# Kernel tuning notes

Hardware: AMD Instinct MI355X
Metric: run time of the kernel (lower is better)

Reference implementation:

```python
import jax, jax.numpy as jnp
import numpy as np

NL, NS, NE = 16, 256, 100   # nlatent, nspatial, n_embd
B, P, T = 2, 2, 12


def _xavier(key, shape):
    # torch xavier_uniform: fan_in = shape[1]*prod(rest), fan_out = shape[0]*prod(rest)
    rf = int(np.prod(shape[2:])) if len(shape) > 2 else 1
    fan_in, fan_out = shape[1] * rf, shape[0] * rf
    b = float(np.sqrt(6.0 / (fan_in + fan_out)))
    return jax.random.uniform(key, shape, jnp.float32, -b, b)


def setup_inputs() -> dict:
    key = jax.random.key(0)
    ks = jax.random.split(key, 8)
    x = jax.random.normal(ks[0], (B, P, T, NL, NS), jnp.float32)
    K = _xavier(ks[1], (NS, NS, NL))
    Q = _xavier(ks[2], (NS, NS, NL))
    V = _xavier(ks[3], (NS, NS, NL))
    Aoo = jnp.ones((NS, NS), jnp.float32)
    # Ann is initialized to zeros in the module; use nonzero values so the
    # clamped geometric recurrence over time is actually exercised.
    Ann = jax.random.uniform(ks[4], (NE,), jnp.float32, -0.9, 0.9)
    Aon = _xavier(ks[5], (NS, NS, NE))
    Ano = _xavier(ks[6], (NS, NS, NE))
    w = jnp.ones((NS,), jnp.float32) / NS
    return {"x": x, "K": K, "Q": Q, "V": V, "Aoo": Aoo,
            "Ann": Ann, "Aon": Aon, "Ano": Ano, "w": w}


def reference(x, K, Q, V, Aoo, Ann, Aon, Ano, w):
    # kvt[B,p,T,X,Y] = sum_{x,c} Q[Y,x,c] K[X,x,c] x[B,p,T,c,x]
    kvt = jnp.einsum('Yxc,Xxc,BpTcx->BpTXY', Q, K, x)
    Aon_c = jnp.clip(Aon, -1.0, 1.0)
    Ano_c = jnp.clip(Ano, -1.0, 1.0)

    # t = T-1 term (elementwise Aoo) and t = T-2 term
    h = Aoo[None, None, None] * kvt[:, :, -1:]
    h = h + jnp.einsum('xyn,XYn,BpTXY->BpTxy', Aon_c, Ano_c, kvt[:, :, -2:-1])

    nT = x.shape[2]
    # Ann sequence used in the loop: A_2 = Ann (raw), A_{j+1} = clip(A_j * Ann)
    def step(a, _):
        return jnp.clip(a * Ann, -1.0, 1.0), a
    _, A_seq = jax.lax.scan(step, Ann, None, length=nT - 2)  # [T-2, n], A_seq[j-2]=A_j

    # loop index j=2..T-1 touches time slice t = T-1-j, i.e. t = T-3 .. 0
    s = jnp.einsum('XYn,BpJXY->BpJn', Ano_c, kvt[:, :, :nT - 2])  # J = t in 0..T-3
    A_t = A_seq[::-1]                       # align A_j with time index t = T-1-j
    s2 = jnp.einsum('Jn,BpJn->Bpn', A_t, s)
    h = h + jnp.einsum('xyn,Bpn->Bpxy', Aon_c, s2)[:, :, None]  # [B,p,1,x,y]

    q = jnp.einsum('Xxc,Bpcx->BpcX', V, x[:, :, -1])
    y = jnp.einsum('x,BpcX,BpTXx->BpTc', w, q, h)  # [B,p,1,c]
    return y
```

## Files before the change

### kernel.cpp

```cpp
#include <hip/hip_runtime.h>
#include <hip/hip_fp16.h>


using f32x4 = __attribute__((ext_vector_type(4))) float;
using half8 = __attribute__((ext_vector_type(8))) _Float16;
using half4 = __attribute__((ext_vector_type(4))) _Float16;

#define KVT_STRIDE 3145728ull
#define KS 4

__device__ inline float clip1(float v) { return fminf(fmaxf(v, -1.f), 1.f); }

__device__ inline half8 mul8(uint4 a, uint4 b) {
    half8 x = __builtin_bit_cast(half8, a);
    half8 y = __builtin_bit_cast(half8, b);
    return x * y;
}

__device__ __forceinline__ void gl_lds16(const void* g, void* l) {
    __builtin_amdgcn_global_load_lds(
        (const __attribute__((address_space(1))) void*)g,
        (__attribute__((address_space(3))) void*)l, 16, 0, 0);
}

__global__ void prep_kernel(const float* __restrict__ K, const float* __restrict__ Q,
                            const float* __restrict__ xin,
                            __half* __restrict__ Kh, __half* __restrict__ Qh,
                            __half* __restrict__ u_t)
{
    int b = blockIdx.x, t = threadIdx.x;
    if (b < 512) {
        bool isK = (b < 256);
        int bb = isK ? b : b - 256;
        size_t base = (size_t)bb * 4096 + t * 16;
        const f32x4* src = (const f32x4*)((isK ? K : Q) + base);
        __half* dst = (isK ? Kh : Qh) + base;
        #pragma unroll
        for (int j = 0; j < 2; ++j) {
            f32x4 v0 = src[j * 2], v1 = src[j * 2 + 1];
            half8 h;
            h[0] = (_Float16)v0.x; h[1] = (_Float16)v0.y;
            h[2] = (_Float16)v0.z; h[3] = (_Float16)v0.w;
            h[4] = (_Float16)v1.x; h[5] = (_Float16)v1.y;
            h[6] = (_Float16)v1.z; h[7] = (_Float16)v1.w;
            *(half8*)(dst + j * 8) = h;
        }
    } else {
        int bt = b - 512;
        const float* src = xin + (size_t)bt * 4096;
        int xx = t;
        half8 lo, hi;
        #pragma unroll
        for (int c = 0; c < 8; ++c)  lo[c] = (_Float16)src[c * 256 + xx];
        #pragma unroll
        for (int c = 0; c < 8; ++c)  hi[c] = (_Float16)src[(c + 8) * 256 + xx];
        half8* dst = (half8*)(u_t + (size_t)bt * 4096 + xx * 16);
        dst[0] = lo; dst[1] = hi;
    }
}

__global__ __launch_bounds__(256, 4) void gemm_kvt(
    const __half* __restrict__ Kh, const __half* __restrict__ Qh,
    const __half* __restrict__ u_t, __half* __restrict__ kvtp)
{
    __shared__ __half As[2][128][32];
    __shared__ __half Bs[2][128][32];
    __shared__ __half u_s[1024];

    int bid = blockIdx.x;
    int work = (bid & 7) * 96 + (bid >> 3);
    int kc = work / 192;
    int rem = work - kc * 192;
    int tile = rem / 48;
    int bt = rem - tile * 48;
    int Xb = (tile >> 1) * 128, Yb = (tile & 1) * 128;
    int kbase = kc * 1024;

    int tid = threadIdx.x;
    if (tid < 128)
        *(uint4*)&u_s[tid * 8] = *(const uint4*)(u_t + (size_t)bt * 4096 + kbase + tid * 8);
    __syncthreads();

    int wave = tid >> 6, lane = tid & 63;

    int arow = tid >> 1;
    int apair = (tid & 1) * 2;
    const __half* gA = Kh + (size_t)(Xb + arow) * 4096 + kbase + apair * 8;
    int aswz = (arow >> 1) & 3;
    int asb0 = ((apair + 0) ^ aswz) << 4;
    int asb1 = ((apair + 1) ^ aswz) << 4;

    int srow = lane >> 2;
    int sk = ((lane & 3) ^ ((srow >> 1) & 3)) << 3;
    const __half* gB = Qh + (size_t)(Yb + wave * 16 + srow) * 4096 + kbase + sk;

    int wr = (wave >> 1) * 64, wc = (wave & 1) * 64;
    int lrow = lane & 15, kg = lane >> 4;
    int fb = (kg * 16) ^ (((lrow >> 1) & 3) << 4);

    f32x4 acc[4][4];
    f32x4 zero = {0.f, 0.f, 0.f, 0.f};
    #pragma unroll
    for (int m = 0; m < 4; ++m)
        #pragma unroll
        for (int n = 0; n < 4; ++n) acc[m][n] = zero;

    #define ISSUE_B(s, buf)                                                    \
        do {                                                                   \
            _Pragma("unroll")                                                  \
            for (int i_ = 0; i_ < 2; ++i_)                                     \
                gl_lds16(gB + (size_t)(i_ * 64) * 4096 + (s) * 32,             \
                         &Bs[buf][i_ * 64 + wave * 16][0]);                    \
        } while (0)

    #define WRITE_A(s, r0, r1, buf)                                            \
        do {                                                                   \
            uint4 uv0 = *(const uint4*)&u_s[(s) * 32 + apair * 8];             \
            uint4 uv1 = *(const uint4*)&u_s[(s) * 32 + apair * 8 + 8];         \
            *(half8*)((char*)&As[buf][arow][0] + asb0) = mul8(r0, uv0);        \
            *(half8*)((char*)&As[buf][arow][0] + asb1) = mul8(r1, uv1);        \
        } while (0)

    #define COMPUTE(cur)                                                       \
        do {                                                                   \
            half8 af[4], bf[4];                                                \
            _Pragma("unroll")                                                  \
            for (int m = 0; m < 4; ++m)                                        \
                af[m] = *(const half8*)((const char*)&As[cur][wr + m * 16 + lrow][0] + fb); \
            _Pragma("unroll")                                                  \
            for (int n = 0; n < 4; ++n)                                        \
                bf[n] = *(const half8*)((const char*)&Bs[cur][wc + n * 16 + lrow][0] + fb); \
            _Pragma("unroll")                                                  \
            for (int m = 0; m < 4; ++m)                                        \
                _Pragma("unroll")                                              \
                for (int n = 0; n < 4; ++n)                                    \
                    acc[m][n] = __builtin_amdgcn_mfma_f32_16x16x32_f16(af[m], bf[n], acc[m][n], 0, 0, 0); \
        } while (0)

    #define STEP(s, c0, c1, i0, i1, cur)                                       \
        do {                                                                   \
            if ((s) < 31) asm volatile("s_waitcnt vmcnt(4) lgkmcnt(0)" ::: "memory"); \
            else          asm volatile("s_waitcnt vmcnt(0) lgkmcnt(0)" ::: "memory"); \
            __builtin_amdgcn_s_barrier();                                      \
            __builtin_amdgcn_sched_barrier(0);                                 \
            COMPUTE(cur);                                                      \
            asm volatile("s_waitcnt lgkmcnt(0)" ::: "memory");                 \
            __builtin_amdgcn_s_barrier();                                      \
            __builtin_amdgcn_sched_barrier(0);                                 \
            if ((s) + 2 < 32) {                                                \
                const __half* a_ = gA + ((s) + 2) * 32;                        \
                i0 = *(const uint4*)a_;                                        \
                i1 = *(const uint4*)(a_ + 8);                                  \
                ISSUE_B((s) + 2, cur);                                         \
            }                                                                  \
            if ((s) + 1 < 32) WRITE_A((s) + 1, c0, c1, (cur) ^ 1);             \
        } while (0)

    uint4 aP0, aP1, aC0, aC1;
    aP0 = *(const uint4*)gA;
    aP1 = *(const uint4*)(gA + 8);
    ISSUE_B(0, 0);
    aC0 = *(const uint4*)(gA + 32);
    aC1 = *(const uint4*)(gA + 40);
    ISSUE_B(1, 1);
    WRITE_A(0, aP0, aP1, 0);

    #pragma unroll
    for (int s = 0; s < 32; s += 2) {
        STEP(s,     aC0, aC1, aP0, aP1, 0);
        STEP(s + 1, aP0, aP1, aC0, aC1, 1);
    }
    #undef STEP
    #undef COMPUTE
    #undef WRITE_A
    #undef ISSUE_B

    __half* outp = kvtp + (size_t)kc * KVT_STRIDE + (size_t)bt * 65536;
    int row0 = Xb + wr + kg * 4;
    int col0 = Yb + wc + lrow;
    #pragma unroll
    for (int m = 0; m < 4; ++m)
        #pragma unroll
        for (int n = 0; n < 4; ++n)
            #pragma unroll
            for (int rr = 0; rr < 4; ++rr)
                outp[(size_t)(row0 + m * 16 + rr) * 256 + col0 + n * 16] =
                    __float2half(acc[m][n][rr]);
}

__global__ __launch_bounds__(256) void mid_kernel(
    const float* __restrict__ Ano, const __half* __restrict__ kvtp,
    const float* __restrict__ V, const float* __restrict__ xin,
    const float* __restrict__ Aon, const float* __restrict__ wv,
    float* __restrict__ Sp, float* __restrict__ R, float* __restrict__ W2p)
{
    __shared__ __align__(16) char smem[75328];
    int b = blockIdx.x, tid = threadIdx.x;

    if (b < 512) {
        float* anoT = (float*)smem;
        float (*kvt_s)[128] = (float(*)[128])(smem + 52800);
        int cb = b;
        int k0 = cb * 128;

        {
            const f32x4* src = (const f32x4*)(Ano + (size_t)k0 * 100);
            for (int i = tid; i < 3200; i += 256) {
                f32x4 f = __builtin_nontemporal_load(src + i);
                int e = i * 4;
                int k = e / 100;
                int n = e - k * 100;
                #pragma unroll
                for (int j = 0; j < 4; ++j) {
                    int nn = n + j, kk2 = k;
                    if (nn >= 100) { nn -= 100; ++kk2; }
                    anoT[nn * 132 + kk2] = clip1(f[j]);
                }
            }
        }
        {
            for (int idx = tid; idx < 5632; idx += 256) {
                int rI = idx >> 7, k = idx & 127;
                int bpr = rI / 11, Jr = rI - bpr * 11;
                size_t off = (size_t)(bpr * 12 + Jr) * 65536 + k0 + k;
                float v = 0.f;
                #pragma unroll
                for (int c = 0; c < KS; ++c)
                    v += __half2float(kvtp[(size_t)c * KVT_STRIDE + off]);
                kvt_s[rI][k] = v;
            }
        }
        __syncthreads();

        int lane = tid & 63;
        int bp = tid >> 6;
        bool has2 = lane < 36;
        float acc0[11], acc1[11];
        #pragma unroll
        for (int J = 0; J < 11; ++J) { acc0[J] = 0.f; acc1[J] = 0.f; }

        const float* a0p = anoT + lane * 132;
        const float* a1p = anoT + (64 + lane) * 132;
        for (int k = 0; k < 128; k += 4) {
            f32x4 kv[11];
            #pragma unroll
            for (int J = 0; J < 11; ++J)
                kv[J] = *(const f32x4*)&kvt_s[bp * 11 + J][k];
            f32x4 a0v = *(const f32x4*)(a0p + k);
            f32x4 a1v = {0.f, 0.f, 0.f, 0.f};
            if (has2) a1v = *(const f32x4*)(a1p + k);
            #pragma unroll
            for (int kk = 0; kk < 4; ++kk) {
                #pragma unroll
                for (int J = 0; J < 11; ++J) {
                    acc0[J] += kv[J][kk] * a0v[kk];
                    acc1[J] += kv[J][kk] * a1v[kk];
                }
            }
        }
        float* outb = Sp + ((size_t)cb * 4 + bp) * 1100;
        #pragma unroll
        for (int J = 0; J < 11; ++J) {
            outb[J * 100 + lane] = acc0[J];
            if (has2) outb[J * 100 + 64 + lane] = acc1[J];
        }
    } else if (b < 768) {
        float* vrow = (float*)smem;
        int X = b - 512;
        {
            const float4* src = (const float4*)(V + (size_t)X * 4096);
            float4* dst = (float4*)vrow;
            for (int i = tid; i < 1024; i += 256) dst[i] = src[i];
        }
        __syncthreads();
        int bp = tid >> 6, c = (tid >> 2) & 15, g = tid & 3;
        const float* xl = xin + ((size_t)(bp * 12) + 11) * 4096 + c * 256;
        float p = 0.f;
        #pragma unroll 4
        for (int x = g * 64; x < g * 64 + 64; ++x)
            p += xl[x] * vrow[x * 16 + c];
        p += __shfl_xor(p, 1);
        p += __shfl_xor(p, 2);
        if (g == 0) R[((size_t)bp * 256 + X) * 16 + c] = p;
    } else {
        int idx = b - 768;
        int X = idx >> 1, h = idx & 1;
        int g = h * 2 + (tid >> 7), n = tid & 127;
        if (n < 100) {
            const float* base = Aon + (size_t)X * 25600 + (size_t)g * 6400 + n;
            float acc = 0.f;
            for (int bb = 0; bb < 64; ++bb)
                acc += wv[g * 64 + bb] * clip1(__builtin_nontemporal_load(base + (size_t)bb * 100));
            W2p[((size_t)g * 256 + X) * 100 + n] = acc;
        }
    }
}

__global__ void reduce_s(const float* __restrict__ Sp, float* __restrict__ Sq,
                         float* __restrict__ out)
{
    int bid = blockIdx.x;
    int t = threadIdx.x;
    if (bid == 0 && t < 64) out[t] = 0.f;
    int qq = bid & 3, idx = bid >> 2;
    int bp = idx / 11, J = idx - bp * 11;
    if (t >= 100) return;
    float acc = 0.f;
    for (int c = qq * 128; c < qq * 128 + 128; ++c)
        acc += Sp[((size_t)c * 4 + bp) * 1100 + J * 100 + t];
    Sq[(size_t)(qq * 44 + idx) * 100 + t] = acc;
}

__global__ __launch_bounds__(256) void hw_kernel(const float* __restrict__ Aoo,
                                                 const float* __restrict__ wv,
                                                 const __half* __restrict__ kvtp,
                                                 const float* __restrict__ W2p,
                                                 const float* __restrict__ Sq,
                                                 const float* __restrict__ Ann,
                                                 const float* __restrict__ R,
                                                 float* __restrict__ out)
{
    __shared__ float yp[4][16];
    __shared__ float c2s[128];
    int bp = blockIdx.x >> 6, Xg = blockIdx.x & 63;
    int tid = threadIdx.x;

    if (tid < 128) {
        int n = tid;
        float r = 0.f;
        if (n < 100) {
            float S[11];
            #pragma unroll
            for (int J = 0; J < 11; ++J) {
                float s = 0.f;
                #pragma unroll
                for (int qq = 0; qq < 4; ++qq)
                    s += Sq[(size_t)(qq * 44 + bp * 11 + J) * 100 + n];
                S[J] = s;
            }
            float a = Ann[n];
            float seq[10];
            float v = a;
            seq[0] = v;
            #pragma unroll
            for (int s2 = 1; s2 < 10; ++s2) { v = clip1(v * a); seq[s2] = v; }
            r = S[10];
            #pragma unroll
            for (int J = 0; J < 10; ++J)
                r += seq[9 - J] * S[J];
        }
        c2s[n] = r;
    }
    __syncthreads();

    int wave = tid >> 6, lane = tid & 63;
    int X = Xg * 4 + wave;
    size_t base = (size_t)(bp * 12 + 11) * 65536 + (size_t)X * 256;
    const float* ao = Aoo + (size_t)X * 256;
    float red = 0.f;
    #pragma unroll
    for (int qq = 0; qq < 4; ++qq) {
        int xx = qq * 64 + lane;
        float kvv = 0.f;
        #pragma unroll
        for (int c = 0; c < KS; ++c)
            kvv += __half2float(kvtp[(size_t)c * KVT_STRIDE + base + xx]);
        red += wv[xx] * ao[xx] * kvv;
    }
    float w2a = 0.f, w2b = 0.f;
    #pragma unroll
    for (int g = 0; g < 4; ++g) {
        w2a += W2p[((size_t)g * 256 + X) * 100 + lane];
        if (lane < 36) w2b += W2p[((size_t)g * 256 + X) * 100 + 64 + lane];
    }
    red += c2s[lane] * w2a;
    if (lane < 36)
        red += c2s[64 + lane] * w2b;
    #pragma unroll
    for (int off = 32; off; off >>= 1) red += __shfl_xor(red, off);
    if (lane < 16) yp[wave][lane] = red * R[((size_t)bp * 256 + X) * 16 + lane];
    __syncthreads();
    if (tid < 16) {
        float s = yp[0][tid] + yp[1][tid] + yp[2][tid] + yp[3][tid];
        atomicAdd(&out[bp * 16 + tid], s);
    }
}

extern "C" void kernel_launch(void* const* d_in, const int* in_sizes, int n_in,
                              void* d_out, int out_size, void* d_ws, size_t ws_size,
                              hipStream_t stream)
{
    const float* x   = (const float*)d_in[0];
    const float* K   = (const float*)d_in[1];
    const float* Q   = (const float*)d_in[2];
    const float* V   = (const float*)d_in[3];
    const float* Aoo = (const float*)d_in[4];
    const float* Ann = (const float*)d_in[5];
    const float* Aon = (const float*)d_in[6];
    const float* Ano = (const float*)d_in[7];
    const float* wv  = (const float*)d_in[8];
    float* out = (float*)d_out;

    char* ws = (char*)d_ws;
    const size_t o_Qh   = 0;
    const size_t o_Kh   = o_Qh + (size_t)2 * 1024 * 1024;
    const size_t o_ut   = o_Kh + (size_t)2 * 1024 * 1024;
    const size_t o_kvtp = o_ut + (size_t)512 * 1024;
    const size_t o_Sp   = o_kvtp + (size_t)KS * KVT_STRIDE * 2;
    const size_t o_Sq   = o_Sp + (size_t)512 * 4400 * 4;
    const size_t o_W2   = o_Sq + (size_t)17600 * 4 + 64;
    const size_t o_R    = o_W2 + (size_t)102400 * 4;

    __half* Qh  = (__half*)(ws + o_Qh);
    __half* Kh  = (__half*)(ws + o_Kh);
    __half* u_t = (__half*)(ws + o_ut);
    __half* kvtp = (__half*)(ws + o_kvtp);
    float* Sp   = (float*)(ws + o_Sp);
    float* Sq   = (float*)(ws + o_Sq);
    float* W2p  = (float*)(ws + o_W2);
    float* R    = (float*)(ws + o_R);

    hipLaunchKernelGGL(prep_kernel, dim3(560),  dim3(256), 0, stream,
                       K, Q, x, Kh, Qh, u_t);
    hipLaunchKernelGGL(gemm_kvt,    dim3(768),  dim3(256), 0, stream, Kh, Qh, u_t, kvtp);
    hipLaunchKernelGGL(mid_kernel,  dim3(1280), dim3(256), 0, stream,
                       Ano, kvtp, V, x, Aon, wv, Sp, R, W2p);
    hipLaunchKernelGGL(reduce_s,    dim3(176),  dim3(128), 0, stream, Sp, Sq, out);
    hipLaunchKernelGGL(hw_kernel,   dim3(256),  dim3(256), 0, stream,
                       Aoo, wv, kvtp, W2p, Sq, Ann, R, out);
}
```

Before: 98.88 us.

## Store clipped Ano as fp16 in LDS, vectorize kvt partial loads, widen reduce split

The mid_kernel now keeps the clipped Ano slice in shared memory as fp16 in its natural [k][n] layout rather than transposing it to fp32. This shrinks LDS use from about 75KB to 49KB so more blocks can be resident, and it removes the scattered transpose stores. The kvt partial-sum loads use 16-byte half8 vector loads across the four split-K partitions instead of scalar half loads. reduce_s now splits over 8 chunks instead of 4, giving twice as many blocks, and hw_kernel sums 8 partials. Keeping Ano in fp16 adds a small precision loss and replaces vector LDS reads with scalar half reads inside the inner loop.

```diff
diff --git a/kernel.cpp b/kernel.cpp
--- a/kernel.cpp
+++ b/kernel.cpp
@@ -194,12 +194,12 @@
     const float* __restrict__ Aon, const float* __restrict__ wv,
     float* __restrict__ Sp, float* __restrict__ R, float* __restrict__ W2p)
 {
-    __shared__ __align__(16) char smem[75328];
+    __shared__ __align__(16) char smem[48960];
     int b = blockIdx.x, tid = threadIdx.x;
 
     if (b < 512) {
-        float* anoT = (float*)smem;
-        float (*kvt_s)[128] = (float(*)[128])(smem + 52800);
+        __half* anoH = (__half*)smem;
+        float (*kvt_s)[132] = (float(*)[132])(smem + 25728);
         int cb = b;
         int k0 = cb * 128;
 
@@ -207,27 +207,29 @@
             const f32x4* src = (const f32x4*)(Ano + (size_t)k0 * 100);
             for (int i = tid; i < 3200; i += 256) {
                 f32x4 f = __builtin_nontemporal_load(src + i);
-                int e = i * 4;
-                int k = e / 100;
-                int n = e - k * 100;
+                half4 h;
+                h[0] = (_Float16)clip1(f.x); h[1] = (_Float16)clip1(f.y);
+                h[2] = (_Float16)clip1(f.z); h[3] = (_Float16)clip1(f.w);
+                *(half4*)&anoH[i * 4] = h;
+            }
+        }
+        {
+            for (int idx = tid; idx < 704; idx += 256) {
+                int rI = idx >> 4, g = idx & 15;
+                int bpr = rI / 11, Jr = rI - bpr * 11;
+                const __half* p = kvtp + (size_t)(bpr * 12 + Jr) * 65536 + k0 + g * 8;
+                half8 v0 = *(const half8*)(p);
+                half8 v1 = *(const half8*)(p + KVT_STRIDE);
+                half8 v2 = *(const half8*)(p + 2 * KVT_STRIDE);
+                half8 v3 = *(const half8*)(p + 3 * KVT_STRIDE);
+                f32x4 lo, hi;
                 #pragma unroll
                 for (int j = 0; j < 4; ++j) {
-                    int nn = n + j, kk2 = k;
-                    if (nn >= 100) { nn -= 100; ++kk2; }
-                    anoT[nn * 132 + kk2] = clip1(f[j]);
+                    lo[j] = (float)v0[j] + (float)v1[j] + (float)v2[j] + (float)v3[j];
+                    hi[j] = (float)v0[j+4] + (float)v1[j+4] + (float)v2[j+4] + (float)v3[j+4];
                 }
-            }
-        }
-        {
-            for (int idx = tid; idx < 5632; idx += 256) {
-                int rI = idx >> 7, k = idx & 127;
-                int bpr = rI / 11, Jr = rI - bpr * 11;
-                size_t off = (size_t)(bpr * 12 + Jr) * 65536 + k0 + k;
-                float v = 0.f;
-                #pragma unroll
-                for (int c = 0; c < KS; ++c)
-                    v += __half2float(kvtp[(size_t)c * KVT_STRIDE + off]);
-                kvt_s[rI][k] = v;
+                *(f32x4*)&kvt_s[rI][g * 8]     = lo;
+                *(f32x4*)&kvt_s[rI][g * 8 + 4] = hi;
             }
         }
         __syncthreads();
@@ -239,22 +241,20 @@
         #pragma unroll
         for (int J = 0; J < 11; ++J) { acc0[J] = 0.f; acc1[J] = 0.f; }
 
-        const float* a0p = anoT + lane * 132;
-        const float* a1p = anoT + (64 + lane) * 132;
         for (int k = 0; k < 128; k += 4) {
             f32x4 kv[11];
             #pragma unroll
             for (int J = 0; J < 11; ++J)
                 kv[J] = *(const f32x4*)&kvt_s[bp * 11 + J][k];
-            f32x4 a0v = *(const f32x4*)(a0p + k);
-            f32x4 a1v = {0.f, 0.f, 0.f, 0.f};
-            if (has2) a1v = *(const f32x4*)(a1p + k);
             #pragma unroll
             for (int kk = 0; kk < 4; ++kk) {
+                float a0 = (float)anoH[(k + kk) * 100 + lane];
+                float a1r = (float)anoH[(k + kk) * 100 + 64 + lane];
+                float a1 = has2 ? a1r : 0.f;
                 #pragma unroll
                 for (int J = 0; J < 11; ++J) {
-                    acc0[J] += kv[J][kk] * a0v[kk];
-                    acc1[J] += kv[J][kk] * a1v[kk];
+                    acc0[J] += kv[J][kk] * a0;
+                    acc1[J] += kv[J][kk] * a1;
                 }
             }
         }
@@ -302,11 +302,11 @@
     int bid = blockIdx.x;
     int t = threadIdx.x;
     if (bid == 0 && t < 64) out[t] = 0.f;
-    int qq = bid & 3, idx = bid >> 2;
+    int qq = bid & 7, idx = bid >> 3;
     int bp = idx / 11, J = idx - bp * 11;
     if (t >= 100) return;
     float acc = 0.f;
-    for (int c = qq * 128; c < qq * 128 + 128; ++c)
+    for (int c = qq * 64; c < qq * 64 + 64; ++c)
         acc += Sp[((size_t)c * 4 + bp) * 1100 + J * 100 + t];
     Sq[(size_t)(qq * 44 + idx) * 100 + t] = acc;
 }
@@ -334,7 +334,7 @@
             for (int J = 0; J < 11; ++J) {
                 float s = 0.f;
                 #pragma unroll
-                for (int qq = 0; qq < 4; ++qq)
+                for (int qq = 0; qq < 8; ++qq)
                     s += Sq[(size_t)(qq * 44 + bp * 11 + J) * 100 + n];
                 S[J] = s;
             }
@@ -408,7 +408,7 @@
     const size_t o_kvtp = o_ut + (size_t)512 * 1024;
     const size_t o_Sp   = o_kvtp + (size_t)KS * KVT_STRIDE * 2;
     const size_t o_Sq   = o_Sp + (size_t)512 * 4400 * 4;
-    const size_t o_W2   = o_Sq + (size_t)17600 * 4 + 64;
+    const size_t o_W2   = o_Sq + (size_t)35200 * 4 + 64;
     const size_t o_R    = o_W2 + (size_t)102400 * 4;
 
     __half* Qh  = (__half*)(ws + o_Qh);
@@ -425,7 +425,7 @@
     hipLaunchKernelGGL(gemm_kvt,    dim3(768),  dim3(256), 0, stream, Kh, Qh, u_t, kvtp);
     hipLaunchKernelGGL(mid_kernel,  dim3(1280), dim3(256), 0, stream,
                        Ano, kvtp, V, x, Aon, wv, Sp, R, W2p);
-    hipLaunchKernelGGL(reduce_s,    dim3(176),  dim3(128), 0, stream, Sp, Sq, out);
+    hipLaunchKernelGGL(reduce_s,    dim3(352),  dim3(128), 0, stream, Sp, Sq, out);
     hipLaunchKernelGGL(hw_kernel,   dim3(256),  dim3(256), 0, stream,
                        Aoo, wv, kvtp, W2p, Sq, Ann, R, out);
 }
```

Measured after the change: 87.84 us. 1.13x faster.
